# Kernel optimization log

Measured on AMD Instinct MI355X. Metric: run time of the kernel, lower is better.

The kernel has to match this reference:

```python
import jax, jax.numpy as jnp
import numpy as np

TARGET = 8000  # __out_target
B, C, F = 16, 256, 16000


def setup_inputs() -> dict:
    key = jax.random.key(0)
    k1, k2 = jax.random.split(key)
    fe = jax.random.normal(k1, (B, C, F), dtype=jnp.float32)
    # face -> collapse-group assignment produced by the sequential edge-collapse;
    # here randomized but in-range [0, TARGET)
    group_ids = jax.random.randint(k2, (B, F), 0, TARGET, dtype=jnp.int64)
    return {"fe": fe, "group_ids": group_ids}


def reference(fe, group_ids):
    # MeshUnion.rebuild_features: pooled feature = mean of member-face features.
    # fe: [B, C, F] float, group_ids: [B, F] int in [0, TARGET)
    def pool_one(fe_m, gid):  # fe_m: [C, F], gid: [F]
        sums = jax.ops.segment_sum(fe_m.T, gid, num_segments=TARGET)  # [TARGET, C]
        cnt = jax.ops.segment_sum(jnp.ones(gid.shape, fe_m.dtype), gid,
                                  num_segments=TARGET)                # [TARGET]
        return (sums / jnp.maximum(cnt, 1.0)[:, None]).T              # [C, TARGET]

    return jax.vmap(pool_one)(fe, group_ids)  # [B, C, TARGET]
```

## Files before the change

### kernel.cpp

```cpp
#include <hip/hip_runtime.h>
#include <stdint.h>


#define NB 16
#define NC 256
#define NF 16000
#define NT 8000
#define CPB 16

typedef unsigned int uint;
typedef unsigned short ushort;
typedef float f32x4 __attribute__((ext_vector_type(4)));

__device__ __forceinline__ float bf2f(uint h) { return __uint_as_float(h << 16); }
__device__ __forceinline__ uint cvtpk(float lo, float hi) {
    uint r;
    asm("v_cvt_pk_bf16_f32 %0, %1, %2" : "=v"(r) : "v"(lo), "v"(hi));
    return r;
}

__global__ __launch_bounds__(256) void hist_kernel(const int* __restrict__ gid,
                                                   int* __restrict__ cnt) {
    int i = blockIdx.x * 256 + threadIdx.x;
    if (i >= NB * NF / 4) return;
    int4 g = ((const int4*)gid)[i];
    int* c = cnt + (i / (NF / 4)) * NT;
    atomicAdd(&c[g.x], 1);
    atomicAdd(&c[g.y], 1);
    atomicAdd(&c[g.z], 1);
    atomicAdd(&c[g.w], 1);
}

__global__ __launch_bounds__(256) void scan_kernel(const int* __restrict__ cnt_g,
                                                   uint* __restrict__ pk,
                                                   uint* __restrict__ cursor) {
    __shared__ int partial[256];
    const int b = blockIdx.x, tid = threadIdx.x;
    const int* cnt = cnt_g + b * NT;

    int loc[32], nv[32];
    int ts = 0;
    if (tid < 250) {
        const int4* c4 = (const int4*)(cnt + 32 * tid);
#pragma unroll
        for (int j = 0; j < 8; ++j) {
            int4 v = c4[j];
            loc[4 * j + 0] = ts; nv[4 * j + 0] = v.x; ts += v.x;
            loc[4 * j + 1] = ts; nv[4 * j + 1] = v.y; ts += v.y;
            loc[4 * j + 2] = ts; nv[4 * j + 2] = v.z; ts += v.z;
            loc[4 * j + 3] = ts; nv[4 * j + 3] = v.w; ts += v.w;
        }
    }
    partial[tid] = (tid < 250) ? ts : 0;
    __syncthreads();

    if (tid < 64) {
        int s0 = partial[4 * tid], s1 = partial[4 * tid + 1];
        int s2 = partial[4 * tid + 2], s3 = partial[4 * tid + 3];
        int lsum = s0 + s1 + s2 + s3;
        int inc = lsum;
        for (int d = 1; d < 64; d <<= 1) {
            int u = __shfl_up(inc, d);
            if (tid >= d) inc += u;
        }
        int exc = inc - lsum;
        partial[4 * tid + 0] = exc;
        partial[4 * tid + 1] = exc + s0;
        partial[4 * tid + 2] = exc + s0 + s1;
        partial[4 * tid + 3] = exc + s0 + s1 + s2;
    }
    __syncthreads();

    if (tid < 250) {
        int base = partial[tid];
        uint* pkb = pk + (size_t)b * NT + 32 * tid;
        uint* cb = cursor + (size_t)b * NT + 32 * tid;
#pragma unroll
        for (int j = 0; j < 32; ++j) {
            uint o = (uint)(base + loc[j]);
            pkb[j] = o | ((uint)nv[j] << 14);
            cb[j] = o;
        }
    }
}

__global__ __launch_bounds__(256) void invperm_kernel(const int* __restrict__ gid,
                                                      uint* __restrict__ cursor,
                                                      ushort* __restrict__ sp) {
    const int b = blockIdx.x >> 4, q = blockIdx.x & 15;
    const int tid = threadIdx.x;
    if (tid >= 250) return;
    const int4* g4 = (const int4*)(gid + (size_t)b * NF + q * 1000);
    uint* cb = cursor + (size_t)b * NT;
    uint2* sp2 = (uint2*)(sp + (size_t)b * NF + q * 1000);
    int4 g = g4[tid];
    uint p0 = atomicAdd(&cb[g.x], 1u);
    uint p1 = atomicAdd(&cb[g.y], 1u);
    uint p2 = atomicAdd(&cb[g.z], 1u);
    uint p3 = atomicAdd(&cb[g.w], 1u);
    sp2[tid] = make_uint2(p0 | (p1 << 16), p2 | (p3 << 16));
}

#define LGKM_BAR() do {                                          \
        asm volatile("s_waitcnt lgkmcnt(0)" ::: "memory");       \
        __builtin_amdgcn_s_barrier();                            \
        __builtin_amdgcn_sched_barrier(0);                       \
    } while (0)

__global__ __launch_bounds__(1024) void pool_kernel(const float* __restrict__ fe,
                                                    const ushort* __restrict__ sp,
                                                    const uint* __restrict__ pk,
                                                    float* __restrict__ out) {
    extern __shared__ char smem[];
    uint* fes32 = (uint*)smem;
    const int bid = blockIdx.x;
    const int b = bid >> 4, cg = bid & 15;
    const int tid = threadIdx.x;
    const size_t bc0 = (size_t)(b * NC + cg * CPB);
    const bool t3 = (tid < 928);
    const bool t8 = (tid < 832);
    const int tl = t3 ? tid + 3072 : tid;

    const uint2* sp2 = (const uint2*)(sp + (size_t)b * NF);
    uint2 s0 = sp2[tid];
    uint2 s1 = sp2[tid + 1024];
    uint2 s2 = sp2[tid + 2048];
    uint2 s3 = sp2[tl];

    const uint* pkb = pk + (size_t)b * NT;
    uint pv[8];
#pragma unroll
    for (int it = 0; it < 7; ++it) pv[it] = pkb[tid + it * 1024];
    pv[7] = 0;
    if (t8) pv[7] = pkb[7168 + tid];

    const f32x4* fe4base = (const f32x4*)(fe + bc0 * NF);
    f32x4 a0, a1, a2, a3, b0, b1, b2, b3;

    {
        const f32x4* fA = fe4base;
        const f32x4* fB = fe4base + (NF / 4);
        a0 = fA[tid]; a1 = fA[tid + 1024]; a2 = fA[tid + 2048]; a3 = fA[tl];
        b0 = fB[tid]; b1 = fB[tid + 1024]; b2 = fB[tid + 2048]; b3 = fB[tl];
    }

#define PAIR_WRITE(F, S, VA, VB) do {                                    \
        (F)[(S).x & 0xFFFFu] = cvtpk((VA)[0], (VB)[0]);                  \
        (F)[(S).x >> 16]     = cvtpk((VA)[1], (VB)[1]);                  \
        (F)[(S).y & 0xFFFFu] = cvtpk((VA)[2], (VB)[2]);                  \
        (F)[(S).y >> 16]     = cvtpk((VA)[3], (VB)[3]);                  \
    } while (0)

#define GATHER_ST(F, P, T) do {                                          \
        uint p_ = (P);                                                   \
        uint off_ = p_ & 0x3FFFu, n_ = p_ >> 14;                         \
        float sa_ = 0.f, sb_ = 0.f;                                      \
        uint r_ = 0;                                                     \
        for (; r_ + 2 <= n_; r_ += 2) {                                  \
            uint2 w_;                                                    \
            __builtin_memcpy(&w_, &(F)[off_ + r_], 8);                   \
            sa_ += bf2f(w_.x & 0xFFFFu) + bf2f(w_.y & 0xFFFFu);          \
            sb_ += bf2f(w_.x >> 16) + bf2f(w_.y >> 16);                  \
        }                                                                \
        if (r_ < n_) {                                                   \
            uint w_ = (F)[off_ + r_];                                    \
            sa_ += bf2f(w_ & 0xFFFFu);                                   \
            sb_ += bf2f(w_ >> 16);                                       \
        }                                                                \
        float rn_ = n_ ? __builtin_amdgcn_rcpf((float)n_) : 0.f;         \
        __builtin_nontemporal_store(sa_ * rn_, &oA[T]);                  \
        __builtin_nontemporal_store(sb_ * rn_, &oB[T]);                  \
    } while (0)

#pragma unroll
    for (int k = 0; k < CPB / 2; ++k) {
        uint* F = fes32 + (k & 1) * 16000;

        PAIR_WRITE(F, s0, a0, b0);
        PAIR_WRITE(F, s1, a1, b1);
        PAIR_WRITE(F, s2, a2, b2);
        if (t3) PAIR_WRITE(F, s3, a3, b3);

        if (k + 1 < CPB / 2) {
            const f32x4* fA = fe4base + (size_t)(2 * k + 2) * (NF / 4);
            const f32x4* fB = fA + (NF / 4);
            a0 = fA[tid]; a1 = fA[tid + 1024]; a2 = fA[tid + 2048]; a3 = fA[tl];
            b0 = fB[tid]; b1 = fB[tid + 1024]; b2 = fB[tid + 2048]; b3 = fB[tl];
        }

        LGKM_BAR();

        float* oA = out + (bc0 + (size_t)(2 * k)) * NT;
        float* oB = out + (bc0 + (size_t)(2 * k + 1)) * NT;
#pragma unroll
        for (int it = 0; it < 7; ++it) GATHER_ST(F, pv[it], tid + it * 1024);
        if (t8) GATHER_ST(F, pv[7], 7168 + tid);
    }
#undef GATHER_ST
#undef PAIR_WRITE
}

__device__ __forceinline__ void lds_fadd(unsigned addr, float v) {
    asm volatile("ds_add_f32 %0, %1" :: "v"(addr), "v"(v));
}
__global__ __launch_bounds__(256) void pool_fused_kernel(const float* __restrict__ fe,
                                                         const int* __restrict__ gid,
                                                         float* __restrict__ out) {
    __shared__ float acc[NT];
    __shared__ int cnt[NT];
    const int bc = blockIdx.x, b = bc >> 8, tid = threadIdx.x;
    for (int t = tid; t < NT; t += 256) { acc[t] = 0.0f; cnt[t] = 0; }
    __syncthreads();
    const unsigned accb = (unsigned)(uintptr_t)acc;
    const float4* fe4 = (const float4*)(fe + (size_t)bc * NF);
    const int4* gid4 = (const int4*)(gid + (size_t)b * NF);
    for (int i = tid; i < NF / 4; i += 256) {
        float4 v = fe4[i];
        int4 g = gid4[i];
        lds_fadd(accb + 4u * (unsigned)g.x, v.x); atomicAdd(&cnt[g.x], 1);
        lds_fadd(accb + 4u * (unsigned)g.y, v.y); atomicAdd(&cnt[g.y], 1);
        lds_fadd(accb + 4u * (unsigned)g.z, v.z); atomicAdd(&cnt[g.z], 1);
        lds_fadd(accb + 4u * (unsigned)g.w, v.w); atomicAdd(&cnt[g.w], 1);
    }
    asm volatile("s_waitcnt lgkmcnt(0)" ::: "memory");
    __syncthreads();
    float* orow = out + (size_t)bc * NT;
    for (int t = tid; t < NT; t += 256) {
        int n = cnt[t];
        orow[t] = acc[t] / (float)(n > 0 ? n : 1);
    }
}

extern "C" void kernel_launch(void* const* d_in, const int* in_sizes, int n_in,
                              void* d_out, int out_size, void* d_ws, size_t ws_size,
                              hipStream_t stream) {
    const float* fe = (const float*)d_in[0];
    const int* gid = (const int*)d_in[1];
    float* out = (float*)d_out;

    const size_t O_CNT = 0;
    const size_t O_CUR = 512000;
    const size_t O_PK  = 1024000;
    const size_t O_SP  = 1536000;
    const size_t TOTAL = 2048000;

    if (ws_size >= TOTAL) {
        char* w = (char*)d_ws;
        int* cnt = (int*)(w + O_CNT);
        uint* cursor = (uint*)(w + O_CUR);
        uint* pk = (uint*)(w + O_PK);
        ushort* sp = (ushort*)(w + O_SP);

        static bool lds_opted = false;
        if (!lds_opted) {
            (void)hipFuncSetAttribute((const void*)pool_kernel,
                                      hipFuncAttributeMaxDynamicSharedMemorySize,
                                      128000);
            lds_opted = true;
        }

        (void)hipMemsetAsync(cnt, 0, 512000, stream);
        hist_kernel<<<(NB * NF / 4 + 255) / 256, 256, 0, stream>>>(gid, cnt);
        scan_kernel<<<NB, 256, 0, stream>>>(cnt, pk, cursor);
        invperm_kernel<<<NB * 16, 256, 0, stream>>>(gid, cursor, sp);
        pool_kernel<<<NB * (NC / CPB), 1024, 128000, stream>>>(fe, sp, pk, out);
    } else {
        pool_fused_kernel<<<NB * NC, 256, 0, stream>>>(fe, gid, out);
    }
}
```

Baseline: 106.6 us.

## Process four channels per LDS pass with interleaved 64-bit bf16 slots

The pool kernel now scatters four channels per iteration into a single LDS buffer, storing two packed bf16 pairs per face slot as 64-bit entries. The gather then reads 128-bit words and accumulates four channels at once, which halves the number of gather passes and pv decode work per channel. Double buffering is replaced by a second barrier after the gather, and two channel pairs of global loads are kept in flight, raising register pressure.

```diff
diff --git a/kernel.cpp b/kernel.cpp
--- a/kernel.cpp
+++ b/kernel.cpp
@@ -112,7 +112,8 @@
                                                     const uint* __restrict__ pk,
                                                     float* __restrict__ out) {
     extern __shared__ char smem[];
-    uint* fes32 = (uint*)smem;
+    uint* fesw = (uint*)smem;
+    const uint2* fes64 = (const uint2*)smem;
     const int bid = blockIdx.x;
     const int b = bid >> 4, cg = bid & 15;
     const int tid = threadIdx.x;
@@ -136,68 +137,86 @@
 
     const f32x4* fe4base = (const f32x4*)(fe + bc0 * NF);
     f32x4 a0, a1, a2, a3, b0, b1, b2, b3;
-
-    {
-        const f32x4* fA = fe4base;
-        const f32x4* fB = fe4base + (NF / 4);
-        a0 = fA[tid]; a1 = fA[tid + 1024]; a2 = fA[tid + 2048]; a3 = fA[tl];
-        b0 = fB[tid]; b1 = fB[tid + 1024]; b2 = fB[tid + 2048]; b3 = fB[tl];
-    }
-
-#define PAIR_WRITE(F, S, VA, VB) do {                                    \
-        (F)[(S).x & 0xFFFFu] = cvtpk((VA)[0], (VB)[0]);                  \
-        (F)[(S).x >> 16]     = cvtpk((VA)[1], (VB)[1]);                  \
-        (F)[(S).y & 0xFFFFu] = cvtpk((VA)[2], (VB)[2]);                  \
-        (F)[(S).y >> 16]     = cvtpk((VA)[3], (VB)[3]);                  \
-    } while (0)
-
-#define GATHER_ST(F, P, T) do {                                          \
-        uint p_ = (P);                                                   \
-        uint off_ = p_ & 0x3FFFu, n_ = p_ >> 14;                         \
-        float sa_ = 0.f, sb_ = 0.f;                                      \
-        uint r_ = 0;                                                     \
-        for (; r_ + 2 <= n_; r_ += 2) {                                  \
-            uint2 w_;                                                    \
-            __builtin_memcpy(&w_, &(F)[off_ + r_], 8);                   \
-            sa_ += bf2f(w_.x & 0xFFFFu) + bf2f(w_.y & 0xFFFFu);          \
-            sb_ += bf2f(w_.x >> 16) + bf2f(w_.y >> 16);                  \
-        }                                                                \
-        if (r_ < n_) {                                                   \
-            uint w_ = (F)[off_ + r_];                                    \
-            sa_ += bf2f(w_ & 0xFFFFu);                                   \
-            sb_ += bf2f(w_ >> 16);                                       \
-        }                                                                \
-        float rn_ = n_ ? __builtin_amdgcn_rcpf((float)n_) : 0.f;         \
-        __builtin_nontemporal_store(sa_ * rn_, &oA[T]);                  \
-        __builtin_nontemporal_store(sb_ * rn_, &oB[T]);                  \
-    } while (0)
-
-#pragma unroll
-    for (int k = 0; k < CPB / 2; ++k) {
-        uint* F = fes32 + (k & 1) * 16000;
-
-        PAIR_WRITE(F, s0, a0, b0);
-        PAIR_WRITE(F, s1, a1, b1);
-        PAIR_WRITE(F, s2, a2, b2);
-        if (t3) PAIR_WRITE(F, s3, a3, b3);
-
-        if (k + 1 < CPB / 2) {
-            const f32x4* fA = fe4base + (size_t)(2 * k + 2) * (NF / 4);
-            const f32x4* fB = fA + (NF / 4);
-            a0 = fA[tid]; a1 = fA[tid + 1024]; a2 = fA[tid + 2048]; a3 = fA[tl];
-            b0 = fB[tid]; b1 = fB[tid + 1024]; b2 = fB[tid + 2048]; b3 = fB[tl];
-        }
+    f32x4 c0, c1, c2, c3, d0, d1, d2, d3;
+
+#define LOADPAIR(CH, X0, X1, X2, X3, Y0, Y1, Y2, Y3) do {               \
+        const f32x4* fX = fe4base + (size_t)(CH) * (NF / 4);            \
+        const f32x4* fY = fX + (NF / 4);                                \
+        X0 = fX[tid]; X1 = fX[tid + 1024];                              \
+        X2 = fX[tid + 2048]; X3 = fX[tl];                               \
+        Y0 = fY[tid]; Y1 = fY[tid + 1024];                              \
+        Y2 = fY[tid + 2048]; Y3 = fY[tl];                               \
+    } while (0)
+
+#define SCAT2(S, VX, VY, IDX) do {                                      \
+        fesw[2u * ((S).x & 0xFFFFu) + (IDX)] = cvtpk((VX)[0], (VY)[0]); \
+        fesw[2u * ((S).x >> 16) + (IDX)]     = cvtpk((VX)[1], (VY)[1]); \
+        fesw[2u * ((S).y & 0xFFFFu) + (IDX)] = cvtpk((VX)[2], (VY)[2]); \
+        fesw[2u * ((S).y >> 16) + (IDX)]     = cvtpk((VX)[3], (VY)[3]); \
+    } while (0)
+
+#define QGATHER(P, T) do {                                              \
+        uint p_ = (P);                                                  \
+        uint off_ = p_ & 0x3FFFu, n_ = p_ >> 14;                        \
+        float g0_ = 0.f, g1_ = 0.f, g2_ = 0.f, g3_ = 0.f;               \
+        uint r_ = 0;                                                    \
+        for (; r_ + 2 <= n_; r_ += 2) {                                 \
+            uint4 w_;                                                   \
+            __builtin_memcpy(&w_, &fes64[off_ + r_], 16);               \
+            g0_ += bf2f(w_.x & 0xFFFFu) + bf2f(w_.z & 0xFFFFu);         \
+            g1_ += bf2f(w_.x >> 16) + bf2f(w_.z >> 16);                 \
+            g2_ += bf2f(w_.y & 0xFFFFu) + bf2f(w_.w & 0xFFFFu);         \
+            g3_ += bf2f(w_.y >> 16) + bf2f(w_.w >> 16);                 \
+        }                                                               \
+        if (r_ < n_) {                                                  \
+            uint2 w_;                                                   \
+            __builtin_memcpy(&w_, &fes64[off_ + r_], 8);                \
+            g0_ += bf2f(w_.x & 0xFFFFu);                                \
+            g1_ += bf2f(w_.x >> 16);                                    \
+            g2_ += bf2f(w_.y & 0xFFFFu);                                \
+            g3_ += bf2f(w_.y >> 16);                                    \
+        }                                                               \
+        float rn_ = n_ ? __builtin_amdgcn_rcpf((float)n_) : 0.f;        \
+        __builtin_nontemporal_store(g0_ * rn_, &oA[T]);                 \
+        __builtin_nontemporal_store(g1_ * rn_, &oB[T]);                 \
+        __builtin_nontemporal_store(g2_ * rn_, &oC[T]);                 \
+        __builtin_nontemporal_store(g3_ * rn_, &oD[T]);                 \
+    } while (0)
+
+    LOADPAIR(0, a0, a1, a2, a3, b0, b1, b2, b3);
+    LOADPAIR(2, c0, c1, c2, c3, d0, d1, d2, d3);
+
+#pragma unroll
+    for (int k = 0; k < 4; ++k) {
+        SCAT2(s0, a0, b0, 0);
+        SCAT2(s1, a1, b1, 0);
+        SCAT2(s2, a2, b2, 0);
+        if (t3) SCAT2(s3, a3, b3, 0);
+        if (k + 1 < 4)
+            LOADPAIR(4 * (k + 1), a0, a1, a2, a3, b0, b1, b2, b3);
+
+        SCAT2(s0, c0, d0, 1);
+        SCAT2(s1, c1, d1, 1);
+        SCAT2(s2, c2, d2, 1);
+        if (t3) SCAT2(s3, c3, d3, 1);
+        if (k + 1 < 4)
+            LOADPAIR(4 * (k + 1) + 2, c0, c1, c2, c3, d0, d1, d2, d3);
 
         LGKM_BAR();
 
-        float* oA = out + (bc0 + (size_t)(2 * k)) * NT;
-        float* oB = out + (bc0 + (size_t)(2 * k + 1)) * NT;
-#pragma unroll
-        for (int it = 0; it < 7; ++it) GATHER_ST(F, pv[it], tid + it * 1024);
-        if (t8) GATHER_ST(F, pv[7], 7168 + tid);
-    }
-#undef GATHER_ST
-#undef PAIR_WRITE
+        float* oA = out + (bc0 + (size_t)(4 * k)) * NT;
+        float* oB = oA + NT;
+        float* oC = oB + NT;
+        float* oD = oC + NT;
+#pragma unroll
+        for (int it = 0; it < 7; ++it) QGATHER(pv[it], tid + it * 1024);
+        if (t8) QGATHER(pv[7], 7168 + tid);
+
+        LGKM_BAR();
+    }
+#undef QGATHER
+#undef SCAT2
+#undef LOADPAIR
 }
 
 __device__ __forceinline__ void lds_fadd(unsigned addr, float v) {
```

Result: slower. 124.7 us (+17.0%).

## Fuse histogram, scan and inverse-permutation into one persistent kernel with grid barriers

Applied to the files above, without the earlier changes.

Replaces the count memset and three preprocessing launches with a single 256-block kernel. The kernel zeroes the counts itself and separates the histogram, per-batch scan and inverse-permutation phases with software grid barriers built on agent-scope atomics. The aim is to remove launch gaps and the large memset ahead of the pooling kernel. In exchange it relies on all 256 blocks being co-resident, and the spin barriers add their own synchronization latency.

```diff
diff --git a/kernel.cpp b/kernel.cpp
--- a/kernel.cpp
+++ b/kernel.cpp
@@ -19,87 +19,120 @@
     return r;
 }
 
-__global__ __launch_bounds__(256) void hist_kernel(const int* __restrict__ gid,
-                                                   int* __restrict__ cnt) {
-    int i = blockIdx.x * 256 + threadIdx.x;
-    if (i >= NB * NF / 4) return;
-    int4 g = ((const int4*)gid)[i];
-    int* c = cnt + (i / (NF / 4)) * NT;
-    atomicAdd(&c[g.x], 1);
-    atomicAdd(&c[g.y], 1);
-    atomicAdd(&c[g.z], 1);
-    atomicAdd(&c[g.w], 1);
-}
-
-__global__ __launch_bounds__(256) void scan_kernel(const int* __restrict__ cnt_g,
-                                                   uint* __restrict__ pk,
-                                                   uint* __restrict__ cursor) {
+
+__device__ __forceinline__ void gbar(uint* bar) {
+    __syncthreads();
+    if (threadIdx.x == 0) {
+        uint old = __hip_atomic_fetch_add(&bar[0], 1u, __ATOMIC_ACQ_REL,
+                                          __HIP_MEMORY_SCOPE_AGENT);
+        if (old == 255u) {
+            __hip_atomic_store(&bar[1], 1u, __ATOMIC_RELEASE,
+                               __HIP_MEMORY_SCOPE_AGENT);
+        } else {
+            while (__hip_atomic_load(&bar[1], __ATOMIC_ACQUIRE,
+                                     __HIP_MEMORY_SCOPE_AGENT) == 0u)
+                __builtin_amdgcn_s_sleep(2);
+        }
+        __threadfence();
+    }
+    __syncthreads();
+}
+
+__global__ __launch_bounds__(256) void preproc_kernel(const int* __restrict__ gid,
+                                                      int* __restrict__ cnt,
+                                                      uint* __restrict__ pk,
+                                                      uint* __restrict__ cursor,
+                                                      ushort* __restrict__ sp,
+                                                      uint* __restrict__ bar) {
     __shared__ int partial[256];
-    const int b = blockIdx.x, tid = threadIdx.x;
-    const int* cnt = cnt_g + b * NT;
-
-    int loc[32], nv[32];
-    int ts = 0;
+    const int blk = blockIdx.x, tid = threadIdx.x;
+
+    {
+        uint* c = (uint*)cnt;
+        int base = blk * 500;
+        __hip_atomic_store(&c[base + tid], 0u, __ATOMIC_RELAXED,
+                           __HIP_MEMORY_SCOPE_AGENT);
+        if (tid < 244)
+            __hip_atomic_store(&c[base + 256 + tid], 0u, __ATOMIC_RELAXED,
+                               __HIP_MEMORY_SCOPE_AGENT);
+    }
+    gbar(bar + 0);
+
     if (tid < 250) {
-        const int4* c4 = (const int4*)(cnt + 32 * tid);
-#pragma unroll
-        for (int j = 0; j < 8; ++j) {
-            int4 v = c4[j];
-            loc[4 * j + 0] = ts; nv[4 * j + 0] = v.x; ts += v.x;
-            loc[4 * j + 1] = ts; nv[4 * j + 1] = v.y; ts += v.y;
-            loc[4 * j + 2] = ts; nv[4 * j + 2] = v.z; ts += v.z;
-            loc[4 * j + 3] = ts; nv[4 * j + 3] = v.w; ts += v.w;
-        }
-    }
-    partial[tid] = (tid < 250) ? ts : 0;
-    __syncthreads();
-
-    if (tid < 64) {
-        int s0 = partial[4 * tid], s1 = partial[4 * tid + 1];
-        int s2 = partial[4 * tid + 2], s3 = partial[4 * tid + 3];
-        int lsum = s0 + s1 + s2 + s3;
-        int inc = lsum;
-        for (int d = 1; d < 64; d <<= 1) {
-            int u = __shfl_up(inc, d);
-            if (tid >= d) inc += u;
-        }
-        int exc = inc - lsum;
-        partial[4 * tid + 0] = exc;
-        partial[4 * tid + 1] = exc + s0;
-        partial[4 * tid + 2] = exc + s0 + s1;
-        partial[4 * tid + 3] = exc + s0 + s1 + s2;
-    }
-    __syncthreads();
+        int i = blk * 250 + tid;
+        int4 g = ((const int4*)gid)[i];
+        int* c = cnt + (i / (NF / 4)) * NT;
+        atomicAdd(&c[g.x], 1);
+        atomicAdd(&c[g.y], 1);
+        atomicAdd(&c[g.z], 1);
+        atomicAdd(&c[g.w], 1);
+    }
+    gbar(bar + 2);
+
+    if (blk < NB) {
+        const int b = blk;
+        const int* cb_ = cnt + b * NT;
+        int loc[32], nv[32];
+        int ts = 0;
+        if (tid < 250) {
+            const int4* c4 = (const int4*)(cb_ + 32 * tid);
+#pragma unroll
+            for (int j = 0; j < 8; ++j) {
+                int4 v = c4[j];
+                loc[4 * j + 0] = ts; nv[4 * j + 0] = v.x; ts += v.x;
+                loc[4 * j + 1] = ts; nv[4 * j + 1] = v.y; ts += v.y;
+                loc[4 * j + 2] = ts; nv[4 * j + 2] = v.z; ts += v.z;
+                loc[4 * j + 3] = ts; nv[4 * j + 3] = v.w; ts += v.w;
+            }
+        }
+        partial[tid] = (tid < 250) ? ts : 0;
+        __syncthreads();
+
+        if (tid < 64) {
+            int s0 = partial[4 * tid], s1 = partial[4 * tid + 1];
+            int s2 = partial[4 * tid + 2], s3 = partial[4 * tid + 3];
+            int lsum = s0 + s1 + s2 + s3;
+            int inc = lsum;
+            for (int d = 1; d < 64; d <<= 1) {
+                int u = __shfl_up(inc, d);
+                if (tid >= d) inc += u;
+            }
+            int exc = inc - lsum;
+            partial[4 * tid + 0] = exc;
+            partial[4 * tid + 1] = exc + s0;
+            partial[4 * tid + 2] = exc + s0 + s1;
+            partial[4 * tid + 3] = exc + s0 + s1 + s2;
+        }
+        __syncthreads();
+
+        if (tid < 250) {
+            int base = partial[tid];
+            uint* pkb = pk + (size_t)b * NT + 32 * tid;
+            uint* cb = cursor + (size_t)b * NT + 32 * tid;
+#pragma unroll
+            for (int j = 0; j < 32; ++j) {
+                uint o = (uint)(base + loc[j]);
+                pkb[j] = o | ((uint)nv[j] << 14);
+                cb[j] = o;
+            }
+        }
+    }
+    gbar(bar + 4);
 
     if (tid < 250) {
-        int base = partial[tid];
-        uint* pkb = pk + (size_t)b * NT + 32 * tid;
-        uint* cb = cursor + (size_t)b * NT + 32 * tid;
-#pragma unroll
-        for (int j = 0; j < 32; ++j) {
-            uint o = (uint)(base + loc[j]);
-            pkb[j] = o | ((uint)nv[j] << 14);
-            cb[j] = o;
-        }
-    }
-}
-
-__global__ __launch_bounds__(256) void invperm_kernel(const int* __restrict__ gid,
-                                                      uint* __restrict__ cursor,
-                                                      ushort* __restrict__ sp) {
-    const int b = blockIdx.x >> 4, q = blockIdx.x & 15;
-    const int tid = threadIdx.x;
-    if (tid >= 250) return;
-    const int4* g4 = (const int4*)(gid + (size_t)b * NF + q * 1000);
-    uint* cb = cursor + (size_t)b * NT;
-    uint2* sp2 = (uint2*)(sp + (size_t)b * NF + q * 1000);
-    int4 g = g4[tid];
-    uint p0 = atomicAdd(&cb[g.x], 1u);
-    uint p1 = atomicAdd(&cb[g.y], 1u);
-    uint p2 = atomicAdd(&cb[g.z], 1u);
-    uint p3 = atomicAdd(&cb[g.w], 1u);
-    sp2[tid] = make_uint2(p0 | (p1 << 16), p2 | (p3 << 16));
-}
+        const int b = blk >> 4, q = blk & 15;
+        const int4* g4 = (const int4*)(gid + (size_t)b * NF + q * 1000);
+        uint* cb = cursor + (size_t)b * NT;
+        uint2* sp2 = (uint2*)(sp + (size_t)b * NF + q * 1000);
+        int4 g = g4[tid];
+        uint p0 = atomicAdd(&cb[g.x], 1u);
+        uint p1 = atomicAdd(&cb[g.y], 1u);
+        uint p2 = atomicAdd(&cb[g.z], 1u);
+        uint p3 = atomicAdd(&cb[g.w], 1u);
+        sp2[tid] = make_uint2(p0 | (p1 << 16), p2 | (p3 << 16));
+    }
+}
+
 
 #define LGKM_BAR() do {                                          \
         asm volatile("s_waitcnt lgkmcnt(0)" ::: "memory");       \
@@ -242,7 +275,8 @@
     const size_t O_CUR = 512000;
     const size_t O_PK  = 1024000;
     const size_t O_SP  = 1536000;
-    const size_t TOTAL = 2048000;
+    const size_t O_BAR = 2048000;
+    const size_t TOTAL = 2048032;
 
     if (ws_size >= TOTAL) {
         char* w = (char*)d_ws;
@@ -250,6 +284,7 @@
         uint* cursor = (uint*)(w + O_CUR);
         uint* pk = (uint*)(w + O_PK);
         ushort* sp = (ushort*)(w + O_SP);
+        uint* bar = (uint*)(w + O_BAR);
 
         static bool lds_opted = false;
         if (!lds_opted) {
@@ -259,10 +294,8 @@
             lds_opted = true;
         }
 
-        (void)hipMemsetAsync(cnt, 0, 512000, stream);
-        hist_kernel<<<(NB * NF / 4 + 255) / 256, 256, 0, stream>>>(gid, cnt);
-        scan_kernel<<<NB, 256, 0, stream>>>(cnt, pk, cursor);
-        invperm_kernel<<<NB * 16, 256, 0, stream>>>(gid, cursor, sp);
+        (void)hipMemsetAsync(bar, 0, 32, stream);
+        preproc_kernel<<<256, 256, 0, stream>>>(gid, cnt, pk, cursor, sp, bar);
         pool_kernel<<<NB * (NC / CPB), 1024, 128000, stream>>>(fe, sp, pk, out);
     } else {
         pool_fused_kernel<<<NB * NC, 256, 0, stream>>>(fe, gid, out);
```

Result: slower. 193.0 us (+81.1%).
